# Optimization experiments

Measured on AMD Instinct MI355X. Metric: run time of the kernel, lower is better.

## Reference

```python
import jax, jax.numpy as jnp
from jax import lax
import numpy as np

P = 1        # padding width
REF0 = 2     # reference rows/cols (ref[0]) -> conv input channels
WP = 3       # window width (ref[1]) -> conv kernel size along border
HID = 8      # hidden channels


def _make_branch(key):
    k = jax.random.split(key, 6)
    s1 = 1.0 / np.sqrt(REF0 * WP)
    s2 = 1.0 / np.sqrt(HID)
    w1 = jax.random.uniform(k[0], (HID, REF0, WP, 1), jnp.float32, -s1, s1)
    b1 = jax.random.uniform(k[1], (HID,), jnp.float32, -s1, s1)
    w2 = jax.random.uniform(k[2], (HID, HID), jnp.float32, -s2, s2)
    b2 = jax.random.uniform(k[3], (HID,), jnp.float32, -s2, s2)
    w3 = jax.random.uniform(k[4], (1, HID), jnp.float32, -s2, s2)
    b3 = jax.random.uniform(k[5], (1,), jnp.float32, -s2, s2)
    return w1, b1, w2, b2, w3, b3


def setup_inputs() -> dict:
    key = jax.random.key(0)
    ks = jax.random.split(key, 5)
    x = jax.random.normal(ks[0], (32, 64, 224, 224), jnp.float32)
    d = {"x": x}
    for j, n in enumerate(["t", "b", "l", "r"]):
        w1, b1, w2, b2, w3, b3 = _make_branch(ks[j + 1])
        d[f"{n}w1"], d[f"{n}b1"] = w1, b1
        d[f"{n}w2"], d[f"{n}b2"] = w2, b2
        d[f"{n}w3"], d[f"{n}b3"] = w3, b3
    return d


def _mlp(s, w1, b1, w2, b2, w3, b3):
    # s: [B, REF0, L, C]  (border rows as channels, spatial = (border length, feature channels))
    y = lax.conv_general_dilated(s, w1, (1, 1), "VALID",
                                 dimension_numbers=("NCHW", "OIHW", "NCHW"))
    y = jax.nn.relu(y + b1[None, :, None, None])          # [B, HID, L-2, C]
    y = jax.nn.relu(jnp.einsum("bhlc,oh->bolc", y, w2) + b2[None, :, None, None])
    y = jax.nn.relu(jnp.einsum("bhlc,oh->bolc", y, w3) + b3[None, :, None, None])
    return y[:, 0]                                        # [B, L-2, C]


def reference(x,
              tw1, tb1, tw2, tb2, tw3, tb3,
              bw1, bb1, bw2, bb2, bw3, bb3,
              lw1, lb1, lw2, lb2, lw3, lb3,
              rw1, rb1, rw2, rb2, rw3, rb3):
    B, C, H, W = x.shape
    p = P
    H2, W2 = H + 2 * p, W + 2 * p
    xp = jnp.zeros((B, C, H2, W2), x.dtype).at[:, :, p:H + p, p:W + p].set(x)
    for i in range(p):  # sequential ring updates (data-dependent recurrence)
        top = jnp.transpose(xp[:, :, p - i:p + REF0 - i, :], (0, 2, 3, 1))  # [B,REF0,W2,C]
        xp = xp.at[:, :, p - 1 - i, 1:W2 - 1].set(
            jnp.transpose(_mlp(top, tw1, tb1, tw2, tb2, tw3, tb3), (0, 2, 1)))
        bot = jnp.transpose(xp[:, :, p + H - REF0 + i:p + H + i, :], (0, 2, 3, 1))
        xp = xp.at[:, :, p + H + i, 1:W2 - 1].set(
            jnp.transpose(_mlp(bot, bw1, bb1, bw2, bb2, bw3, bb3), (0, 2, 1)))
        left = jnp.transpose(xp[:, :, :, p - i:p + REF0 - i], (0, 3, 2, 1))  # [B,REF0,H2,C]
        xp = xp.at[:, :, 1:H2 - 1, p - 1 - i].set(
            jnp.transpose(_mlp(left, lw1, lb1, lw2, lb2, lw3, lb3), (0, 2, 1)))
        right = jnp.transpose(xp[:, :, :, p + W - REF0 + i:p + W + i], (0, 3, 2, 1))
        xp = xp.at[:, :, 1:H2 - 1, p + W + i].set(
            jnp.transpose(_mlp(right, rw1, rb1, rw2, rb2, rw3, rb3), (0, 2, 1)))
    return xp
```

## Files before the change

kernel.cpp:

```cpp
#include <hip/hip_runtime.h>

#define BB   32
#define CC   64
#define HH   224
#define WW   224
#define H2   226
#define W2   226
#define HID  8

constexpr unsigned XHW   = HH * WW;
constexpr unsigned HW2   = H2 * W2;
constexpr unsigned NTOT  = BB * CC * HW2;
constexpr unsigned NTOT4 = NTOT / 4;
constexpr unsigned NBORD = BB * CC * HH;

__global__ __launch_bounds__(256) void pad_copy_k(const float* __restrict__ x,
                                                  float* __restrict__ out) {
    unsigned tid = blockIdx.x * 256u + threadIdx.x;
    if (tid >= NTOT4) return;
    unsigned e  = tid * 4u;
    unsigned w  = e % W2;
    unsigned t  = e / W2;
    unsigned h  = t % H2;
    unsigned bc = t / H2;
    float v[4];
#pragma unroll
    for (int j = 0; j < 4; ++j) {
        unsigned hi = h - 1u;
        unsigned wi = w - 1u;
        v[j] = (hi < (unsigned)HH && wi < (unsigned)WW)
                   ? x[bc * XHW + hi * (unsigned)WW + wi]
                   : 0.f;
        ++w;
        if (w == W2) { w = 0; ++h; if (h == H2) { h = 0; ++bc; } }
    }
    reinterpret_cast<float4*>(out)[tid] = make_float4(v[0], v[1], v[2], v[3]);
}

__device__ __forceinline__ float mlp_eval(const float s[2][3],
                                          const float* __restrict__ W1,
                                          const float* __restrict__ B1,
                                          const float* __restrict__ W2m,
                                          const float* __restrict__ B2,
                                          const float* __restrict__ W3,
                                          float b3) {
    float y1[HID];
#pragma unroll
    for (int h = 0; h < HID; ++h) {
        float a = B1[h];
#pragma unroll
        for (int r = 0; r < 2; ++r)
#pragma unroll
            for (int k = 0; k < 3; ++k)
                a = fmaf(s[r][k], W1[h * 6 + r * 3 + k], a);
        y1[h] = fmaxf(a, 0.f);
    }
    float y2[HID];
#pragma unroll
    for (int o = 0; o < HID; ++o) {
        float a = B2[o];
#pragma unroll
        for (int h = 0; h < HID; ++h) a = fmaf(y1[h], W2m[o * 8 + h], a);
        y2[o] = fmaxf(a, 0.f);
    }
    float a = b3;
#pragma unroll
    for (int h = 0; h < HID; ++h) a = fmaf(y2[h], W3[h], a);
    return fmaxf(a, 0.f);
}

__device__ __forceinline__ void load_wts(int t,
                                         const float* w1, const float* b1,
                                         const float* w2, const float* b2,
                                         const float* w3, const float* b3,
                                         float* W1, float* B1, float* W2m,
                                         float* B2, float* W3, float* B3) {
    if (t < 48) W1[t] = w1[t];
    if (t < 64) W2m[t] = w2[t];
    if (t < 8) {
        B1[t] = b1[t];
        B2[t] = b2[t];
        W3[t] = w3[t];
    }
    if (t == 0) B3[0] = b3[0];
}

__global__ __launch_bounds__(256) void border_tb_k(
    const float* __restrict__ x, float* __restrict__ out,
    const float* tw1, const float* tb1, const float* tw2, const float* tb2,
    const float* tw3, const float* tb3,
    const float* bw1, const float* bb1, const float* bw2, const float* bb2,
    const float* bw3, const float* bb3) {
    const bool top = (blockIdx.y == 0);
    const float* w1 = top ? tw1 : bw1;
    const float* b1 = top ? tb1 : bb1;
    const float* w2 = top ? tw2 : bw2;
    const float* b2 = top ? tb2 : bb2;
    const float* w3 = top ? tw3 : bw3;
    const float* b3 = top ? tb3 : bb3;

    __shared__ float W1[48], B1[8], W2m[64], B2[8], W3[8], B3[1];
    load_wts(threadIdx.x, w1, b1, w2, b2, w3, b3, W1, B1, W2m, B2, W3, B3);
    __syncthreads();

    unsigned gid = blockIdx.x * 256u + threadIdx.x;
    if (gid >= NBORD) return;
    unsigned l  = gid % (unsigned)HH;
    unsigned bc = gid / (unsigned)HH;

    const unsigned r0 = top ? 0u : (unsigned)(HH - 2);
    float s[2][3];
#pragma unroll
    for (int r = 0; r < 2; ++r)
#pragma unroll
        for (int k = 0; k < 3; ++k) {
            unsigned xc = l + (unsigned)k - 1u;
            s[r][k] = (xc < (unsigned)WW)
                          ? x[bc * XHW + (r0 + (unsigned)r) * (unsigned)WW + xc]
                          : 0.f;
        }
    float res = mlp_eval(s, W1, B1, W2m, B2, W3, B3[0]);
    unsigned orow = top ? 0u : (unsigned)(H2 - 1);
    out[bc * HW2 + orow * (unsigned)W2 + (l + 1u)] = res;
}

__global__ __launch_bounds__(256) void border_lr_k(
    float* __restrict__ out,
    const float* lw1, const float* lb1, const float* lw2, const float* lb2,
    const float* lw3, const float* lb3,
    const float* rw1, const float* rb1, const float* rw2, const float* rb2,
    const float* rw3, const float* rb3) {
    const bool left = (blockIdx.y == 0);
    const float* w1 = left ? lw1 : rw1;
    const float* b1 = left ? lb1 : rb1;
    const float* w2 = left ? lw2 : rw2;
    const float* b2 = left ? lb2 : rb2;
    const float* w3 = left ? lw3 : rw3;
    const float* b3 = left ? lb3 : rb3;

    __shared__ float W1[48], B1[8], W2m[64], B2[8], W3[8], B3[1];
    load_wts(threadIdx.x, w1, b1, w2, b2, w3, b3, W1, B1, W2m, B2, W3, B3);
    __syncthreads();

    unsigned gid = blockIdx.x * 256u + threadIdx.x;
    if (gid >= NBORD) return;
    unsigned l  = gid % (unsigned)HH;
    unsigned bc = gid / (unsigned)HH;

    const unsigned cbase = left ? 1u : (unsigned)(W2 - 3);
    float s[2][3];
#pragma unroll
    for (int r = 0; r < 2; ++r)
#pragma unroll
        for (int k = 0; k < 3; ++k)
            s[r][k] = out[bc * HW2 + (l + (unsigned)k) * (unsigned)W2 +
                          (cbase + (unsigned)r)];
    float res = mlp_eval(s, W1, B1, W2m, B2, W3, B3[0]);
    unsigned ocol = left ? 0u : (unsigned)(W2 - 1);
    out[bc * HW2 + (l + 1u) * (unsigned)W2 + ocol] = res;
}

extern "C" void kernel_launch(void* const* d_in, const int* in_sizes, int n_in,
                              void* d_out, int out_size, void* d_ws,
                              size_t ws_size, hipStream_t stream) {
    const float* x = (const float*)d_in[0];
    const float* tw[6]; const float* bw[6]; const float* lw[6]; const float* rw[6];
    for (int i = 0; i < 6; ++i) {
        tw[i] = (const float*)d_in[1 + i];
        bw[i] = (const float*)d_in[7 + i];
        lw[i] = (const float*)d_in[13 + i];
        rw[i] = (const float*)d_in[19 + i];
    }
    float* out = (float*)d_out;

    {
        unsigned blocks = (NTOT4 + 255u) / 256u;
        pad_copy_k<<<dim3(blocks), dim3(256), 0, stream>>>(x, out);
    }
    {
        unsigned blocks = (NBORD + 255u) / 256u;
        border_tb_k<<<dim3(blocks, 2), dim3(256), 0, stream>>>(
            x, out, tw[0], tw[1], tw[2], tw[3], tw[4], tw[5],
            bw[0], bw[1], bw[2], bw[3], bw[4], bw[5]);
    }
    {
        unsigned blocks = (NBORD + 255u) / 256u;
        border_lr_k<<<dim3(blocks, 2), dim3(256), 0, stream>>>(
            out, lw[0], lw[1], lw[2], lw[3], lw[4], lw[5],
            rw[0], rw[1], rw[2], rw[3], rw[4], rw[5]);
    }
}
```

Baseline: 207.2 us.

## Fuse padding copy and all four border MLPs into one per-plane kernel

Replaces the three launches (pad copy, top/bottom border, left/right border) with one kernel, using one block per (batch, channel) plane. Each block copies the interior with float4 reads from x and computes the top and bottom rows. It stages the two columns nearest each side in shared memory, so the left/right MLPs read LDS instead of doing strided global reads of the output. The aim is to remove launch overhead, the extra border traffic and the scalar gather in the old copy. The trade-off is that the float4 stores into the padded plane are not 16-byte aligned, and a block of 256 threads now covers a whole plane.

```diff
diff --git a/kernel.cpp b/kernel.cpp
--- a/kernel.cpp
+++ b/kernel.cpp
@@ -8,42 +8,19 @@
 #define W2   226
 #define HID  8
 
-constexpr unsigned XHW   = HH * WW;
-constexpr unsigned HW2   = H2 * W2;
-constexpr unsigned NTOT  = BB * CC * HW2;
-constexpr unsigned NTOT4 = NTOT / 4;
-constexpr unsigned NBORD = BB * CC * HH;
-
-__global__ __launch_bounds__(256) void pad_copy_k(const float* __restrict__ x,
-                                                  float* __restrict__ out) {
-    unsigned tid = blockIdx.x * 256u + threadIdx.x;
-    if (tid >= NTOT4) return;
-    unsigned e  = tid * 4u;
-    unsigned w  = e % W2;
-    unsigned t  = e / W2;
-    unsigned h  = t % H2;
-    unsigned bc = t / H2;
-    float v[4];
-#pragma unroll
-    for (int j = 0; j < 4; ++j) {
-        unsigned hi = h - 1u;
-        unsigned wi = w - 1u;
-        v[j] = (hi < (unsigned)HH && wi < (unsigned)WW)
-                   ? x[bc * XHW + hi * (unsigned)WW + wi]
-                   : 0.f;
-        ++w;
-        if (w == W2) { w = 0; ++h; if (h == H2) { h = 0; ++bc; } }
-    }
-    reinterpret_cast<float4*>(out)[tid] = make_float4(v[0], v[1], v[2], v[3]);
-}
+constexpr unsigned NPLANE = BB * CC;
+constexpr unsigned XHW    = HH * WW;
+constexpr unsigned HW2    = H2 * W2;
+constexpr unsigned F4PP   = HH * (WW/4);
 
 __device__ __forceinline__ float mlp_eval(const float s[2][3],
-                                          const float* __restrict__ W1,
-                                          const float* __restrict__ B1,
-                                          const float* __restrict__ W2m,
-                                          const float* __restrict__ B2,
-                                          const float* __restrict__ W3,
-                                          float b3) {
+                                          const float* __restrict__ W) {
+    const float* W1 = W;
+    const float* B1 = W + 48;
+    const float* W2m = W + 56;
+    const float* B2 = W + 120;
+    const float* W3 = W + 128;
+    const float  b3 = W[136];
     float y1[HID];
 #pragma unroll
     for (int h = 0; h < HID; ++h) {
@@ -69,124 +46,122 @@
     return fmaxf(a, 0.f);
 }
 
-__device__ __forceinline__ void load_wts(int t,
-                                         const float* w1, const float* b1,
-                                         const float* w2, const float* b2,
-                                         const float* w3, const float* b3,
-                                         float* W1, float* B1, float* W2m,
-                                         float* B2, float* W3, float* B3) {
-    if (t < 48) W1[t] = w1[t];
-    if (t < 64) W2m[t] = w2[t];
-    if (t < 8) {
-        B1[t] = b1[t];
-        B2[t] = b2[t];
-        W3[t] = w3[t];
-    }
-    if (t == 0) B3[0] = b3[0];
-}
+#define LOADW(br, pw1, pb1, pw2, pb2, pw3, pb3)                         \
+    if (t < 48) wts[br][t] = pw1[t];                                    \
+    if (t < 64) wts[br][56 + t] = pw2[t];                               \
+    if (t < 8) {                                                        \
+        wts[br][48 + t]  = pb1[t];                                      \
+        wts[br][120 + t] = pb2[t];                                      \
+        wts[br][128 + t] = pw3[t];                                      \
+    }                                                                   \
+    if (t == 0) wts[br][136] = pb3[0];
 
-__global__ __launch_bounds__(256) void border_tb_k(
+__global__ __launch_bounds__(256) void fused_pad_k(
     const float* __restrict__ x, float* __restrict__ out,
     const float* tw1, const float* tb1, const float* tw2, const float* tb2,
     const float* tw3, const float* tb3,
     const float* bw1, const float* bb1, const float* bw2, const float* bb2,
-    const float* bw3, const float* bb3) {
-    const bool top = (blockIdx.y == 0);
-    const float* w1 = top ? tw1 : bw1;
-    const float* b1 = top ? tb1 : bb1;
-    const float* w2 = top ? tw2 : bw2;
-    const float* b2 = top ? tb2 : bb2;
-    const float* w3 = top ? tw3 : bw3;
-    const float* b3 = top ? tb3 : bb3;
-
-    __shared__ float W1[48], B1[8], W2m[64], B2[8], W3[8], B3[1];
-    load_wts(threadIdx.x, w1, b1, w2, b2, w3, b3, W1, B1, W2m, B2, W3, B3);
-    __syncthreads();
-
-    unsigned gid = blockIdx.x * 256u + threadIdx.x;
-    if (gid >= NBORD) return;
-    unsigned l  = gid % (unsigned)HH;
-    unsigned bc = gid / (unsigned)HH;
-
-    const unsigned r0 = top ? 0u : (unsigned)(HH - 2);
-    float s[2][3];
-#pragma unroll
-    for (int r = 0; r < 2; ++r)
-#pragma unroll
-        for (int k = 0; k < 3; ++k) {
-            unsigned xc = l + (unsigned)k - 1u;
-            s[r][k] = (xc < (unsigned)WW)
-                          ? x[bc * XHW + (r0 + (unsigned)r) * (unsigned)WW + xc]
-                          : 0.f;
-        }
-    float res = mlp_eval(s, W1, B1, W2m, B2, W3, B3[0]);
-    unsigned orow = top ? 0u : (unsigned)(H2 - 1);
-    out[bc * HW2 + orow * (unsigned)W2 + (l + 1u)] = res;
-}
-
-__global__ __launch_bounds__(256) void border_lr_k(
-    float* __restrict__ out,
+    const float* bw3, const float* bb3,
     const float* lw1, const float* lb1, const float* lw2, const float* lb2,
     const float* lw3, const float* lb3,
     const float* rw1, const float* rb1, const float* rw2, const float* rb2,
     const float* rw3, const float* rb3) {
-    const bool left = (blockIdx.y == 0);
-    const float* w1 = left ? lw1 : rw1;
-    const float* b1 = left ? lb1 : rb1;
-    const float* w2 = left ? lw2 : rw2;
-    const float* b2 = left ? lb2 : rb2;
-    const float* w3 = left ? lw3 : rw3;
-    const float* b3 = left ? lb3 : rb3;
+    const unsigned bc = blockIdx.x;
+    const unsigned t  = threadIdx.x;
 
-    __shared__ float W1[48], B1[8], W2m[64], B2[8], W3[8], B3[1];
-    load_wts(threadIdx.x, w1, b1, w2, b2, w3, b3, W1, B1, W2m, B2, W3, B3);
+    __shared__ float wts[4][137];
+    __shared__ float Lcol[H2][2];
+    __shared__ float Rcol[H2][2];
+
+    LOADW(0, tw1, tb1, tw2, tb2, tw3, tb3)
+    LOADW(1, bw1, bb1, bw2, bb2, bw3, bb3)
+    LOADW(2, lw1, lb1, lw2, lb2, lw3, lb3)
+    LOADW(3, rw1, rb1, rw2, rb2, rw3, rb3)
     __syncthreads();
 
-    unsigned gid = blockIdx.x * 256u + threadIdx.x;
-    if (gid >= NBORD) return;
-    unsigned l  = gid % (unsigned)HH;
-    unsigned bc = gid / (unsigned)HH;
+    const float* xp = x + (size_t)bc * XHW;
+    float*       op = out + (size_t)bc * HW2;
 
-    const unsigned cbase = left ? 1u : (unsigned)(W2 - 3);
-    float s[2][3];
+    if (t < HH) {
+        const unsigned l = t;
+        float s[2][3];
 #pragma unroll
-    for (int r = 0; r < 2; ++r)
+        for (int r = 0; r < 2; ++r)
 #pragma unroll
-        for (int k = 0; k < 3; ++k)
-            s[r][k] = out[bc * HW2 + (l + (unsigned)k) * (unsigned)W2 +
-                          (cbase + (unsigned)r)];
-    float res = mlp_eval(s, W1, B1, W2m, B2, W3, B3[0]);
-    unsigned ocol = left ? 0u : (unsigned)(W2 - 1);
-    out[bc * HW2 + (l + 1u) * (unsigned)W2 + ocol] = res;
+            for (int k = 0; k < 3; ++k) {
+                unsigned xc = l + (unsigned)k - 1u;
+                s[r][k] = (xc < (unsigned)WW) ? xp[r * WW + xc] : 0.f;
+            }
+        float tres = mlp_eval(s, wts[0]);
+        op[l + 1u] = tres;
+        if (l < 2u)        Lcol[0][l] = tres;
+        if (l >= HH - 2u)  Rcol[0][l - (HH - 2u)] = tres;
+#pragma unroll
+        for (int r = 0; r < 2; ++r)
+#pragma unroll
+            for (int k = 0; k < 3; ++k) {
+                unsigned xc = l + (unsigned)k - 1u;
+                s[r][k] = (xc < (unsigned)WW) ? xp[(HH - 2u + r) * WW + xc] : 0.f;
+            }
+        float bres = mlp_eval(s, wts[1]);
+        op[(H2 - 1u) * W2 + l + 1u] = bres;
+        if (l < 2u)        Lcol[H2 - 1][l] = bres;
+        if (l >= HH - 2u)  Rcol[H2 - 1][l - (HH - 2u)] = bres;
+    } else if (t == 255u) {
+        op[0]                       = 0.f;
+        op[W2 - 1]                  = 0.f;
+        op[(H2 - 1u) * W2]          = 0.f;
+        op[(H2 - 1u) * W2 + W2 - 1] = 0.f;
+    }
+
+    for (unsigned f = t; f < F4PP; f += 256u) {
+        const unsigned h = f / 56u;
+        const unsigned j = f % 56u;
+        const float4 v = *reinterpret_cast<const float4*>(xp + h * WW + 4u * j);
+        *reinterpret_cast<float4*>(op + (h + 1u) * W2 + 1u + 4u * j) = v;
+        if (j == 0u) {
+            Lcol[h + 1u][0] = v.x;
+            Lcol[h + 1u][1] = v.y;
+        } else if (j == 55u) {
+            Rcol[h + 1u][0] = v.z;
+            Rcol[h + 1u][1] = v.w;
+        }
+    }
+
+    __syncthreads();
+
+    for (unsigned idx = t; idx < 2u * HH; idx += 256u) {
+        const unsigned side = idx / (unsigned)HH;
+        const unsigned l    = idx % (unsigned)HH;
+        float s[2][3];
+        if (side == 0u) {
+#pragma unroll
+            for (int r = 0; r < 2; ++r)
+#pragma unroll
+                for (int k = 0; k < 3; ++k) s[r][k] = Lcol[l + (unsigned)k][r];
+            op[(l + 1u) * W2] = mlp_eval(s, wts[2]);
+        } else {
+#pragma unroll
+            for (int r = 0; r < 2; ++r)
+#pragma unroll
+                for (int k = 0; k < 3; ++k) s[r][k] = Rcol[l + (unsigned)k][r];
+            op[(l + 1u) * W2 + (W2 - 1u)] = mlp_eval(s, wts[3]);
+        }
+    }
 }
 
 extern "C" void kernel_launch(void* const* d_in, const int* in_sizes, int n_in,
                               void* d_out, int out_size, void* d_ws,
                               size_t ws_size, hipStream_t stream) {
     const float* x = (const float*)d_in[0];
-    const float* tw[6]; const float* bw[6]; const float* lw[6]; const float* rw[6];
-    for (int i = 0; i < 6; ++i) {
-        tw[i] = (const float*)d_in[1 + i];
-        bw[i] = (const float*)d_in[7 + i];
-        lw[i] = (const float*)d_in[13 + i];
-        rw[i] = (const float*)d_in[19 + i];
-    }
+    const float* w[24];
+    for (int i = 0; i < 24; ++i) w[i] = (const float*)d_in[1 + i];
     float* out = (float*)d_out;
 
-    {
-        unsigned blocks = (NTOT4 + 255u) / 256u;
-        pad_copy_k<<<dim3(blocks), dim3(256), 0, stream>>>(x, out);
-    }
-    {
-        unsigned blocks = (NBORD + 255u) / 256u;
-        border_tb_k<<<dim3(blocks, 2), dim3(256), 0, stream>>>(
-            x, out, tw[0], tw[1], tw[2], tw[3], tw[4], tw[5],
-            bw[0], bw[1], bw[2], bw[3], bw[4], bw[5]);
-    }
-    {
-        unsigned blocks = (NBORD + 255u) / 256u;
-        border_lr_k<<<dim3(blocks, 2), dim3(256), 0, stream>>>(
-            out, lw[0], lw[1], lw[2], lw[3], lw[4], lw[5],
-            rw[0], rw[1], rw[2], rw[3], rw[4], rw[5]);
-    }
+    fused_pad_k<<<dim3(NPLANE), dim3(256), 0, stream>>>(
+        x, out,
+        w[0], w[1], w[2], w[3], w[4], w[5],
+        w[6], w[7], w[8], w[9], w[10], w[11],
+        w[12], w[13], w[14], w[15], w[16], w[17],
+        w[18], w[19], w[20], w[21], w[22], w[23]);
 }
```

After: 372.5 us. 79.8% more time.
